# Kernel optimization log

Measured on AMD Instinct MI355X. Metric: run time of the kernel, lower is better.

Reference implementation:

```python
import jax, jax.numpy as jnp
import numpy as np

N = 8192        # num_nodes
H = 128         # h_dim
E = 131072      # num edges (avg degree 16)
NREL = 90       # num relations
NB = 8          # num_bases (block-diagonal decomposition)
SI = H // NB    # block size 16


def setup_inputs() -> dict:
    key = jax.random.key(0)
    ks = jax.random.split(key, 24)
    sc = 0.01
    n = lambda k, shape, s=sc: jax.random.normal(k, shape, dtype=jnp.float32) * s
    return {
        'node_ids': jnp.arange(N, dtype=jnp.int32),
        'src': jax.random.randint(ks[0], (E,), 0, N, dtype=jnp.int32),
        'dst': jax.random.randint(ks[1], (E,), 0, N, dtype=jnp.int32),
        'etypes': jax.random.randint(ks[2], (E,), 0, NREL, dtype=jnp.int32),
        'norm': jax.random.uniform(ks[3], (E, 1), dtype=jnp.float32),
        'eps': jax.random.normal(ks[4], (N, H), dtype=jnp.float32),
        # input embedding layer
        'embedding': n(ks[5], (N, H)),
        # RelGraphConv layer 0 ('bdd'): per-relation block-diag weights, self-loop, bias
        'W0': n(ks[6], (NREL, NB, SI, SI)),
        'loop0': n(ks[7], (H, H)),
        'b0': jnp.zeros((H,), jnp.float32),
        # RelGraphConv layer 1
        'W1': n(ks[8], (NREL, NB, SI, SI)),
        'loop1': n(ks[9], (H, H)),
        'b1': jnp.zeros((H,), jnp.float32),
        # z_layer: Linear(H, 2H)  (weights stored as (in, out))
        'Wz': n(ks[10], (H, 2 * H)),
        'bz': jnp.zeros((2 * H,), jnp.float32),
        # inter_layer (UpdateLayer): Linear(H, H) + h_bias
        'Wi': n(ks[11], (H, H)),
        'bi': jnp.zeros((H,), jnp.float32),
        'hbi': jnp.zeros((H,), jnp.float32),
        # output_layer (second UpdateLayer)
        'Wo': n(ks[12], (H, H)),
        'bo': jnp.zeros((H,), jnp.float32),
        'hbo': jnp.zeros((H,), jnp.float32),
    }


def _rgcn_bdd(h, W, loop_w, bias, src, dst, etypes, norm, act):
    # gather src features, split into NB blocks of size SI
    x = h[src].reshape(-1, NB, SI)                       # [E, NB, SI]
    Wg = W[etypes]                                       # [E, NB, SI, SI] per-edge relation block weights
    msg = jnp.einsum('ebi,ebio->ebo', x, Wg).reshape(-1, H) * norm  # [E, H]
    agg = jax.ops.segment_sum(msg, dst, num_segments=N)  # scatter-add to dst
    out = agg + bias + h @ loop_w                        # self-loop + bias
    return act(out) if act is not None else out


def reference(node_ids, src, dst, etypes, norm, eps, embedding,
              W0, loop0, b0, W1, loop1, b1,
              Wz, bz, Wi, bi, hbi, Wo, bo, hbo):
    # input layer: embedding lookup; saved as input_embed
    x0 = embedding[node_ids]                             # [N, H]
    h = _rgcn_bdd(x0, W0, loop0, b0, src, dst, etypes, norm, jax.nn.relu)
    h = _rgcn_bdd(h, W1, loop1, b1, src, dst, etypes, norm, None)
    # VAE head: z ~ N(mean, exp(log_std))
    zml = h @ Wz + bz                                    # [N, 2H]
    z_mean, z_log_std = jnp.split(zml, 2, axis=-1)
    z = z_mean + jnp.exp(z_log_std) * eps                # reparameterized sample
    # decode 1: outer-product reconstruction + fused update
    R = z @ z.T                                          # [N, N]
    h = R @ (z @ Wi + bi) + R @ x0 + hbi
    # decode 2
    R2 = h @ h.T                                         # [N, N]
    out = R2 @ (h @ Wo + bo) + R2 @ x0 + hbo
    return out
```

## Files before the change

kernel.cpp:

```cpp
#include <hip/hip_runtime.h>
#include <hip/hip_bf16.h>
#include <math.h>

#define Hdim 128
#define NBq 8
#define SIq 16

typedef __attribute__((ext_vector_type(8))) short short8x;
typedef __attribute__((ext_vector_type(4))) float f32x4;

__device__ inline unsigned short f2b(float f) {
  unsigned int u = __float_as_uint(f);
  return (unsigned short)((u + 0x7fffu + ((u >> 16) & 1u)) >> 16);
}
__device__ inline unsigned int pack2(float lo, float hi) {
  return (unsigned int)f2b(lo) | ((unsigned int)f2b(hi) << 16);
}

__global__ void k_gather(const float* __restrict__ emb, const int* __restrict__ ids,
                         float* __restrict__ x0, int N) {
  int idx = blockIdx.x * blockDim.x + threadIdx.x;
  int total = N * (Hdim / 4);
  if (idx >= total) return;
  int n  = idx / (Hdim / 4);
  int c4 = idx - n * (Hdim / 4);
  int s  = ids[n];
  ((float4*)x0)[(size_t)n * (Hdim / 4) + c4] =
      ((const float4*)emb)[(size_t)s * (Hdim / 4) + c4];
}

__global__ void k_wtb(const float* __restrict__ Wa, unsigned short* __restrict__ Wta,
                      const float* __restrict__ Wb, unsigned short* __restrict__ Wtb) {
  int rb = blockIdx.x;
  const float* W = blockIdx.y ? Wb : Wa;
  unsigned short* Wt = blockIdx.y ? Wtb : Wta;
  int t = threadIdx.x;
  int i = t >> 4, o = t & 15;
  Wt[(size_t)rb * 256 + o * 16 + i] = f2b(W[(size_t)rb * 256 + i * 16 + o]);
}

__global__ void k_wtt(const float* __restrict__ l0, const float* __restrict__ l1,
                      const float* __restrict__ Wi, const float* __restrict__ Wo,
                      const float* __restrict__ Wz,
                      unsigned short* __restrict__ l0t, unsigned short* __restrict__ l1t,
                      unsigned short* __restrict__ Wit, unsigned short* __restrict__ Wot,
                      unsigned short* __restrict__ Wzt) {
  int idx = blockIdx.x * blockDim.x + threadIdx.x;
  if (idx < 65536) {
    int w = idx >> 14, local = idx & 16383;
    const float* in = (w == 0) ? l0 : (w == 1) ? l1 : (w == 2) ? Wi : Wo;
    unsigned short* out = (w == 0) ? l0t : (w == 1) ? l1t : (w == 2) ? Wit : Wot;
    int n = local >> 7, k = local & 127;
    out[local] = f2b(in[k * 128 + n]);
  } else {
    int local = idx - 65536;
    int n = local >> 7, k = local & 127;
    Wzt[local] = f2b(Wz[k * 256 + n]);
  }
}

__global__ void k_hist(const int* __restrict__ dst, int* __restrict__ cnt, int E) {
  int e = blockIdx.x * blockDim.x + threadIdx.x;
  if (e < E) atomicAdd(&cnt[dst[e]], 1);
}

__global__ __launch_bounds__(1024) void k_scan(const int* __restrict__ cnt,
                                               int* __restrict__ off,
                                               int* __restrict__ cur, int N, int E) {
  __shared__ int part[1024];
  int t = threadIdx.x;
  int ipt = N / 1024;
  int base = t * ipt;
  int loc[8];
  int s = 0;
  for (int i = 0; i < ipt; ++i) { loc[i] = s; s += cnt[base + i]; }
  part[t] = s;
  __syncthreads();
  for (int d = 1; d < 1024; d <<= 1) {
    int v = part[t];
    int add = (t >= d) ? part[t - d] : 0;
    __syncthreads();
    part[t] = v + add;
    __syncthreads();
  }
  int pre = (t == 0) ? 0 : part[t - 1];
  for (int i = 0; i < ipt; ++i) {
    int o = pre + loc[i];
    off[base + i] = o;
    cur[base + i] = o;
  }
  if (t == 0) off[N] = E;
}

__global__ void k_scatter(const int* __restrict__ src, const int* __restrict__ dst,
                          const int* __restrict__ et, const float* __restrict__ norm,
                          int* __restrict__ cur, int* __restrict__ psrc,
                          int* __restrict__ pet, float* __restrict__ pnorm, int E) {
  int e = blockIdx.x * blockDim.x + threadIdx.x;
  if (e >= E) return;
  int p = atomicAdd(&cur[dst[e]], 1);
  psrc[p] = src[e];
  pet[p]  = et[e];
  pnorm[p] = norm[e];
}

#define BF_LO(u) __uint_as_float((u) << 16)
#define BF_HI(u) __uint_as_float((u) & 0xffff0000u)
__global__ __launch_bounds__(128) void k_edge4(
    const float* __restrict__ h, const unsigned short* __restrict__ Wt,
    const int* __restrict__ off, const int* __restrict__ psrc,
    const int* __restrict__ pet, const float* __restrict__ pnorm,
    float* __restrict__ agg) {
  int n = blockIdx.x;
  int f = threadIdx.x;
  int b = f >> 4, o = f & 15;
  int j0 = off[n], j1 = off[n + 1];
  __shared__ float xs[8][Hdim];
  float acc = 0.f;
  for (int j = j0; j < j1; j += 8) {
    int m = min(8, j1 - j);
    for (int q = 0; q < m; ++q)
      xs[q][f] = h[(size_t)psrc[j + q] * Hdim + f];
    __syncthreads();
    for (int q = 0; q < m; ++q) {
      int r = pet[j + q];
      float nv = pnorm[j + q];
      const uint4* wp = (const uint4*)(Wt + ((size_t)r * NBq + b) * 256 + o * 16);
      uint4 wa = wp[0], wb = wp[1];
      const float4* xp = (const float4*)(&xs[q][b * SIq]);
      float4 x0 = xp[0], x1 = xp[1], x2 = xp[2], x3 = xp[3];
      float a = x0.x*BF_LO(wa.x) + x0.y*BF_HI(wa.x) + x0.z*BF_LO(wa.y) + x0.w*BF_HI(wa.y)
              + x1.x*BF_LO(wa.z) + x1.y*BF_HI(wa.z) + x1.z*BF_LO(wa.w) + x1.w*BF_HI(wa.w)
              + x2.x*BF_LO(wb.x) + x2.y*BF_HI(wb.x) + x2.z*BF_LO(wb.y) + x2.w*BF_HI(wb.y)
              + x3.x*BF_LO(wb.z) + x3.y*BF_HI(wb.z) + x3.z*BF_LO(wb.w) + x3.w*BF_HI(wb.w);
      acc = fmaf(a, nv, acc);
    }
    __syncthreads();
  }
  agg[(size_t)n * Hdim + f] = acc;
}

__global__ __launch_bounds__(256) void k_bgemm(
    const float* __restrict__ A, const unsigned short* __restrict__ Bt,
    const float* __restrict__ Gsrc, float* __restrict__ C,
    const float* __restrict__ addm, const float* __restrict__ bias,
    int M, int Nc, int relu, float* __restrict__ gzero) {
  __shared__ unsigned short Al[32][136];
  __shared__ unsigned short Bl[64][136];
  int t = threadIdx.x;
  int bm = blockIdx.x * 32, bn = blockIdx.y * 64;
  if (gzero && blockIdx.x == 0 && blockIdx.y == 0) {
#pragma unroll
    for (int i = 0; i < 16; ++i)
      ((float4*)gzero)[t + 256 * i] = make_float4(0.f, 0.f, 0.f, 0.f);
  }
  {
    int r = t >> 3, c0 = (t & 7) << 4;
    const float4* ap = (const float4*)(A + (size_t)(bm + r) * Hdim + c0);
    float4 a0 = ap[0], a1 = ap[1], a2 = ap[2], a3 = ap[3];
    uint4 p0 = { pack2(a0.x, a0.y), pack2(a0.z, a0.w), pack2(a1.x, a1.y), pack2(a1.z, a1.w) };
    uint4 p1 = { pack2(a2.x, a2.y), pack2(a2.z, a2.w), pack2(a3.x, a3.y), pack2(a3.z, a3.w) };
    *(uint4*)&Al[r][c0]     = p0;
    *(uint4*)&Al[r][c0 + 8] = p1;
  }
  if (Bt) {
    int n = t >> 2, k0 = (t & 3) << 5;
    const uint4* bp = (const uint4*)(Bt + (size_t)(bn + n) * Hdim + k0);
    uint4 b0 = bp[0], b1 = bp[1], b2 = bp[2], b3 = bp[3];
    *(uint4*)&Bl[n][k0]      = b0;
    *(uint4*)&Bl[n][k0 + 8]  = b1;
    *(uint4*)&Bl[n][k0 + 16] = b2;
    *(uint4*)&Bl[n][k0 + 24] = b3;
  } else {
    int n = t & 63, kb = (t >> 6) << 5;
    for (int i = 0; i < 32; ++i) {
      int k = kb + i;
      Bl[n][k] = f2b(Gsrc[(size_t)k * 128 + bn + n]);
    }
  }
  __syncthreads();
  int wv = t >> 6, ln = t & 63;
  int mt = wv & 1;
  int nt0 = (wv >> 1) << 1;
  int lm = ln & 15, lk = ln >> 4;
  f32x4 acc0 = {0.f, 0.f, 0.f, 0.f}, acc1 = {0.f, 0.f, 0.f, 0.f};
#pragma unroll
  for (int ks = 0; ks < 4; ++ks) {
    short8x af = *(const short8x*)&Al[mt * 16 + lm][ks * 32 + lk * 8];
    short8x bf0 = *(const short8x*)&Bl[nt0 * 16 + lm][ks * 32 + lk * 8];
    short8x bf1 = *(const short8x*)&Bl[(nt0 + 1) * 16 + lm][ks * 32 + lk * 8];
    acc0 = __builtin_amdgcn_mfma_f32_16x16x32_bf16(af, bf0, acc0, 0, 0, 0);
    acc1 = __builtin_amdgcn_mfma_f32_16x16x32_bf16(af, bf1, acc1, 0, 0, 0);
  }
  int gcol0 = bn + nt0 * 16 + lm;
  int gcol1 = gcol0 + 16;
  float b0v = bias ? bias[gcol0] : 0.f;
  float b1v = bias ? bias[gcol1] : 0.f;
#pragma unroll
  for (int reg = 0; reg < 4; ++reg) {
    int grow = bm + mt * 16 + lk * 4 + reg;
    size_t o0 = (size_t)grow * Nc + gcol0;
    size_t o1 = (size_t)grow * Nc + gcol1;
    float v0 = acc0[reg] + b0v;
    float v1 = acc1[reg] + b1v;
    if (addm) { v0 += addm[o0]; v1 += addm[o1]; }
    if (relu) { v0 = fmaxf(v0, 0.f); v1 = fmaxf(v1, 0.f); }
    C[o0] = v0;
    C[o1] = v1;
  }
}


__global__ __launch_bounds__(256) void k_bgemm_z(
    const float* __restrict__ A, const unsigned short* __restrict__ Wzt,
    const float* __restrict__ bz, const float* __restrict__ eps,
    float* __restrict__ Z, int M) {
  __shared__ unsigned short Al[32][136];
  __shared__ unsigned short Bm[64][136];
  __shared__ unsigned short Bl[64][136];
  int t = threadIdx.x;
  int bm = blockIdx.x * 32, bn = blockIdx.y * 64;
  {
    int r = t >> 3, c0 = (t & 7) << 4;
    const float4* ap = (const float4*)(A + (size_t)(bm + r) * Hdim + c0);
    float4 a0 = ap[0], a1 = ap[1], a2 = ap[2], a3 = ap[3];
    uint4 p0 = { pack2(a0.x, a0.y), pack2(a0.z, a0.w), pack2(a1.x, a1.y), pack2(a1.z, a1.w) };
    uint4 p1 = { pack2(a2.x, a2.y), pack2(a2.z, a2.w), pack2(a3.x, a3.y), pack2(a3.z, a3.w) };
    *(uint4*)&Al[r][c0]     = p0;
    *(uint4*)&Al[r][c0 + 8] = p1;
  }
  {
    int n = t >> 2, k0 = (t & 3) << 5;
    const uint4* mp = (const uint4*)(Wzt + (size_t)(bn + n) * Hdim + k0);
    const uint4* lp = (const uint4*)(Wzt + (size_t)(bn + 128 + n) * Hdim + k0);
    uint4 m0 = mp[0], m1 = mp[1], m2 = mp[2], m3 = mp[3];
    uint4 l0 = lp[0], l1 = lp[1], l2 = lp[2], l3 = lp[3];
    *(uint4*)&Bm[n][k0]      = m0; *(uint4*)&Bm[n][k0 + 8]  = m1;
    *(uint4*)&Bm[n][k0 + 16] = m2; *(uint4*)&Bm[n][k0 + 24] = m3;
    *(uint4*)&Bl[n][k0]      = l0; *(uint4*)&Bl[n][k0 + 8]  = l1;
    *(uint4*)&Bl[n][k0 + 16] = l2; *(uint4*)&Bl[n][k0 + 24] = l3;
  }
  __syncthreads();
  int wv = t >> 6, ln = t & 63;
  int mt = wv & 1;
  int nt0 = (wv >> 1) << 1;
  int lm = ln & 15, lk = ln >> 4;
  f32x4 am0 = {0,0,0,0}, am1 = {0,0,0,0}, al0 = {0,0,0,0}, al1 = {0,0,0,0};
#pragma unroll
  for (int ks = 0; ks < 4; ++ks) {
    short8x af = *(const short8x*)&Al[mt * 16 + lm][ks * 32 + lk * 8];
    short8x bm0 = *(const short8x*)&Bm[nt0 * 16 + lm][ks * 32 + lk * 8];
    short8x bm1 = *(const short8x*)&Bm[(nt0 + 1) * 16 + lm][ks * 32 + lk * 8];
    short8x bl0 = *(const short8x*)&Bl[nt0 * 16 + lm][ks * 32 + lk * 8];
    short8x bl1 = *(const short8x*)&Bl[(nt0 + 1) * 16 + lm][ks * 32 + lk * 8];
    am0 = __builtin_amdgcn_mfma_f32_16x16x32_bf16(af, bm0, am0, 0, 0, 0);
    am1 = __builtin_amdgcn_mfma_f32_16x16x32_bf16(af, bm1, am1, 0, 0, 0);
    al0 = __builtin_amdgcn_mfma_f32_16x16x32_bf16(af, bl0, al0, 0, 0, 0);
    al1 = __builtin_amdgcn_mfma_f32_16x16x32_bf16(af, bl1, al1, 0, 0, 0);
  }
  int gcol0 = bn + nt0 * 16 + lm;
  int gcol1 = gcol0 + 16;
  float bm0v = bz[gcol0], bm1v = bz[gcol1];
  float bl0v = bz[128 + gcol0], bl1v = bz[128 + gcol1];
#pragma unroll
  for (int reg = 0; reg < 4; ++reg) {
    int grow = bm + mt * 16 + lk * 4 + reg;
    size_t o0 = (size_t)grow * Hdim + gcol0;
    size_t o1 = (size_t)grow * Hdim + gcol1;
    Z[o0] = am0[reg] + bm0v + expf(al0[reg] + bl0v) * eps[o0];
    Z[o1] = am1[reg] + bm1v + expf(al1[reg] + bl1v) * eps[o1];
  }
}

__global__ __launch_bounds__(256) void k_xty(const float* __restrict__ X,
                                             const float* __restrict__ Y,
                                             float* __restrict__ G, int N) {
  __shared__ float xs[8][64];
  __shared__ float ys[8][64];
  int t  = threadIdx.x;
  int tx = t & 15, ty = t >> 4;
  int qr = blockIdx.y >> 1, qc = blockIdx.y & 1;
  int KC = N / gridDim.x;
  int k0 = blockIdx.x * KC;
  int m  = t >> 7, li = t & 127;
  int lr = li >> 4, lc = (li & 15) << 2;
  const float* S = m ? Y : X;
  int coff = (m ? qc : qr) * 64;
  float acc[4][4] = {};
  for (int kb = 0; kb < KC; kb += 8) {
    float4 v = *(const float4*)(S + (size_t)(k0 + kb + lr) * Hdim + coff + lc);
    __syncthreads();
    if (m) *(float4*)&ys[lr][lc] = v; else *(float4*)&xs[lr][lc] = v;
    __syncthreads();
#pragma unroll
    for (int kk = 0; kk < 8; ++kk) {
      float4 xv = *(const float4*)&xs[kk][ty << 2];
      float4 yv = *(const float4*)&ys[kk][tx << 2];
      acc[0][0] += xv.x * yv.x; acc[0][1] += xv.x * yv.y; acc[0][2] += xv.x * yv.z; acc[0][3] += xv.x * yv.w;
      acc[1][0] += xv.y * yv.x; acc[1][1] += xv.y * yv.y; acc[1][2] += xv.y * yv.z; acc[1][3] += xv.y * yv.w;
      acc[2][0] += xv.z * yv.x; acc[2][1] += xv.z * yv.y; acc[2][2] += xv.z * yv.z; acc[2][3] += xv.z * yv.w;
      acc[3][0] += xv.w * yv.x; acc[3][1] += xv.w * yv.y; acc[3][2] += xv.w * yv.z; acc[3][3] += xv.w * yv.w;
    }
  }
  int grow = qr * 64 + (ty << 2);
  int gcol = qc * 64 + (tx << 2);
#pragma unroll
  for (int r = 0; r < 4; ++r)
#pragma unroll
    for (int c = 0; c < 4; ++c)
      atomicAdd(&G[(size_t)(grow + r) * Hdim + gcol + c], acc[r][c]);
}

extern "C" void kernel_launch(void* const* d_in, const int* in_sizes, int n_in,
                              void* d_out, int out_size, void* d_ws, size_t ws_size,
                              hipStream_t stream) {
  const int*   node_ids = (const int*)d_in[0];
  const int*   src      = (const int*)d_in[1];
  const int*   dst      = (const int*)d_in[2];
  const int*   et       = (const int*)d_in[3];
  const float* norm     = (const float*)d_in[4];
  const float* eps      = (const float*)d_in[5];
  const float* emb      = (const float*)d_in[6];
  const float* W0       = (const float*)d_in[7];
  const float* loop0    = (const float*)d_in[8];
  const float* b0       = (const float*)d_in[9];
  const float* W1       = (const float*)d_in[10];
  const float* loop1    = (const float*)d_in[11];
  const float* b1       = (const float*)d_in[12];
  const float* Wz       = (const float*)d_in[13];
  const float* bz       = (const float*)d_in[14];
  const float* Wi       = (const float*)d_in[15];
  const float* bi       = (const float*)d_in[16];
  const float* hbi      = (const float*)d_in[17];
  const float* Wo       = (const float*)d_in[18];
  const float* bo       = (const float*)d_in[19];
  const float* hbo      = (const float*)d_in[20];
  float* out = (float*)d_out;

  const int N  = in_sizes[0];
  const int E  = in_sizes[1];
  const int RB = in_sizes[7] / (SIq * SIq);

  char* ws = (char*)d_ws;
  const size_t MB = 1u << 20;
  const size_t KB = 1u << 10;
  float* X0   = (float*)(ws + 0 * MB);
  float* B1p  = (float*)(ws + 4 * MB);
  float* B2p  = (float*)(ws + 8 * MB);
  float* AGG  = (float*)(ws + 12 * MB);
  float* B3p  = (float*)(ws + 16 * MB);
  float* G    = (float*)(ws + 20 * MB);
  int*   offp = (int*)(ws + 20 * MB + 256 * KB);
  int*   curp = (int*)(ws + 20 * MB + 512 * KB);
  int*   cntp = (int*)(ws + 20 * MB + 768 * KB);
  int*   psrc = (int*)(ws + 21 * MB);
  int*   pet  = (int*)(ws + 21 * MB + 512 * KB);
  float* pnrm = (float*)(ws + 22 * MB);
  unsigned short* Wt0 = (unsigned short*)(ws + 22 * MB + 512 * KB);
  unsigned short* Wt1 = (unsigned short*)(ws + 23 * MB);
  unsigned short* l0t = (unsigned short*)(ws + 24 * MB);
  unsigned short* l1t = (unsigned short*)(ws + 24 * MB + 64 * KB);
  unsigned short* Wit = (unsigned short*)(ws + 24 * MB + 128 * KB);
  unsigned short* Wot = (unsigned short*)(ws + 24 * MB + 192 * KB);
  unsigned short* Wzt = (unsigned short*)(ws + 24 * MB + 256 * KB);

  dim3 blk(256);

  hipMemsetAsync(cntp, 0, (size_t)N * sizeof(int), stream);
  k_hist<<<dim3((E + 255) / 256), blk, 0, stream>>>(dst, cntp, E);
  k_scan<<<dim3(1), dim3(1024), 0, stream>>>(cntp, offp, curp, N, E);
  k_scatter<<<dim3((E + 255) / 256), blk, 0, stream>>>(src, dst, et, norm, curp,
                                                       psrc, pet, pnrm, E);
  k_wtb<<<dim3(RB, 2), blk, 0, stream>>>(W0, Wt0, W1, Wt1);
  k_wtt<<<dim3(384), blk, 0, stream>>>(loop0, loop1, Wi, Wo, Wz, l0t, l1t, Wit, Wot, Wzt);

  k_gather<<<dim3((N * (Hdim / 4) + 255) / 256), blk, 0, stream>>>(emb, node_ids, X0, N);
  k_edge4<<<dim3(N), dim3(128), 0, stream>>>(X0, Wt0, offp, psrc, pet, pnrm, AGG);
  k_bgemm<<<dim3(N / 32, 2), blk, 0, stream>>>(X0, l0t, nullptr, B1p, AGG, b0, N, Hdim, 1, nullptr);
  k_edge4<<<dim3(N), dim3(128), 0, stream>>>(B1p, Wt1, offp, psrc, pet, pnrm, AGG);
  k_bgemm<<<dim3(N / 32, 2), blk, 0, stream>>>(B1p, l1t, nullptr, B2p, AGG, b1, N, Hdim, 0, nullptr);
  k_bgemm_z<<<dim3(N / 32, 2), blk, 0, stream>>>(B2p, Wzt, bz, eps, B1p, N);
  k_bgemm<<<dim3(N / 32, 2), blk, 0, stream>>>(B1p, Wit, nullptr, B3p, X0, bi, N, Hdim, 0, G);
  k_xty<<<dim3(32, 4), blk, 0, stream>>>(B1p, B3p, G, N);
  k_bgemm<<<dim3(N / 32, 2), blk, 0, stream>>>(B1p, nullptr, G, B2p, nullptr, hbi, N, Hdim, 0, nullptr);
  k_bgemm<<<dim3(N / 32, 2), blk, 0, stream>>>(B2p, Wot, nullptr, B3p, X0, bo, N, Hdim, 0, G);
  k_xty<<<dim3(32, 4), blk, 0, stream>>>(B2p, B3p, G, N);
  k_bgemm<<<dim3(N / 32, 2), blk, 0, stream>>>(B2p, nullptr, G, out, nullptr, hbo, N, Hdim, 0, nullptr);
}
```

Baseline: 302.8 us.

## Fuse preprocessing kernels and software-pipeline edge aggregation without shared memory

```diff
diff --git a/kernel.cpp b/kernel.cpp
--- a/kernel.cpp
+++ b/kernel.cpp
@@ -17,51 +17,48 @@
   return (unsigned int)f2b(lo) | ((unsigned int)f2b(hi) << 16);
 }
 
-__global__ void k_gather(const float* __restrict__ emb, const int* __restrict__ ids,
-                         float* __restrict__ x0, int N) {
-  int idx = blockIdx.x * blockDim.x + threadIdx.x;
-  int total = N * (Hdim / 4);
-  if (idx >= total) return;
-  int n  = idx / (Hdim / 4);
-  int c4 = idx - n * (Hdim / 4);
-  int s  = ids[n];
-  ((float4*)x0)[(size_t)n * (Hdim / 4) + c4] =
-      ((const float4*)emb)[(size_t)s * (Hdim / 4) + c4];
-}
-
-__global__ void k_wtb(const float* __restrict__ Wa, unsigned short* __restrict__ Wta,
-                      const float* __restrict__ Wb, unsigned short* __restrict__ Wtb) {
-  int rb = blockIdx.x;
-  const float* W = blockIdx.y ? Wb : Wa;
-  unsigned short* Wt = blockIdx.y ? Wtb : Wta;
-  int t = threadIdx.x;
-  int i = t >> 4, o = t & 15;
-  Wt[(size_t)rb * 256 + o * 16 + i] = f2b(W[(size_t)rb * 256 + i * 16 + o]);
-}
-
-__global__ void k_wtt(const float* __restrict__ l0, const float* __restrict__ l1,
-                      const float* __restrict__ Wi, const float* __restrict__ Wo,
-                      const float* __restrict__ Wz,
-                      unsigned short* __restrict__ l0t, unsigned short* __restrict__ l1t,
-                      unsigned short* __restrict__ Wit, unsigned short* __restrict__ Wot,
-                      unsigned short* __restrict__ Wzt) {
-  int idx = blockIdx.x * blockDim.x + threadIdx.x;
-  if (idx < 65536) {
-    int w = idx >> 14, local = idx & 16383;
-    const float* in = (w == 0) ? l0 : (w == 1) ? l1 : (w == 2) ? Wi : Wo;
-    unsigned short* out = (w == 0) ? l0t : (w == 1) ? l1t : (w == 2) ? Wit : Wot;
-    int n = local >> 7, k = local & 127;
-    out[local] = f2b(in[k * 128 + n]);
+__global__ __launch_bounds__(256) void k_pre(
+    const float* __restrict__ emb, const int* __restrict__ ids, float* __restrict__ x0,
+    const float* __restrict__ W0, unsigned short* __restrict__ Wt0,
+    const float* __restrict__ W1, unsigned short* __restrict__ Wt1, int w0elems,
+    const float* __restrict__ l0, const float* __restrict__ l1,
+    const float* __restrict__ Wi, const float* __restrict__ Wo, const float* __restrict__ Wz,
+    unsigned short* __restrict__ l0t, unsigned short* __restrict__ l1t,
+    unsigned short* __restrict__ Wit, unsigned short* __restrict__ Wot,
+    unsigned short* __restrict__ Wzt,
+    const int* __restrict__ dst, int* __restrict__ cnt, int E,
+    int b1, int b2, int b3) {
+  int bx = blockIdx.x, t = threadIdx.x;
+  if (bx < b1) {
+    int idx = bx * 256 + t;
+    int n = idx >> 5, c4 = idx & 31;
+    int s = ids[n];
+    ((float4*)x0)[(size_t)n * 32 + c4] = ((const float4*)emb)[(size_t)s * 32 + c4];
+  } else if (bx < b2) {
+    int idx = (bx - b1) * 256 + t;
+    const float* W = (idx < w0elems) ? W0 : W1;
+    unsigned short* Wt = (idx < w0elems) ? Wt0 : Wt1;
+    int local = (idx < w0elems) ? idx : idx - w0elems;
+    int rb = local >> 8, io = local & 255;
+    int i = io >> 4, o = io & 15;
+    Wt[(size_t)rb * 256 + o * 16 + i] = f2b(W[(size_t)rb * 256 + i * 16 + o]);
+  } else if (bx < b3) {
+    int idx = (bx - b2) * 256 + t;
+    if (idx < 65536) {
+      int w = idx >> 14, local = idx & 16383;
+      const float* in = (w == 0) ? l0 : (w == 1) ? l1 : (w == 2) ? Wi : Wo;
+      unsigned short* out = (w == 0) ? l0t : (w == 1) ? l1t : (w == 2) ? Wit : Wot;
+      int n = local >> 7, k = local & 127;
+      out[local] = f2b(in[k * 128 + n]);
+    } else {
+      int local = idx - 65536;
+      int n = local >> 7, k = local & 127;
+      Wzt[local] = f2b(Wz[k * 256 + n]);
+    }
   } else {
-    int local = idx - 65536;
-    int n = local >> 7, k = local & 127;
-    Wzt[local] = f2b(Wz[k * 256 + n]);
-  }
-}
-
-__global__ void k_hist(const int* __restrict__ dst, int* __restrict__ cnt, int E) {
-  int e = blockIdx.x * blockDim.x + threadIdx.x;
-  if (e < E) atomicAdd(&cnt[dst[e]], 1);
+    int e = (bx - b3) * 256 + t;
+    if (e < E) atomicAdd(&cnt[dst[e]], 1);
+  }
 }
 
 __global__ __launch_bounds__(1024) void k_scan(const int* __restrict__ cnt,
@@ -106,36 +103,44 @@
 
 #define BF_LO(u) __uint_as_float((u) << 16)
 #define BF_HI(u) __uint_as_float((u) & 0xffff0000u)
-__global__ __launch_bounds__(128) void k_edge4(
+__global__ __launch_bounds__(256) void k_edge6(
     const float* __restrict__ h, const unsigned short* __restrict__ Wt,
     const int* __restrict__ off, const int* __restrict__ psrc,
     const int* __restrict__ pet, const float* __restrict__ pnorm,
     float* __restrict__ agg) {
-  int n = blockIdx.x;
-  int f = threadIdx.x;
+  int t = threadIdx.x;
+  int n = blockIdx.x * 2 + (t >> 7);
+  int f = t & 127;
   int b = f >> 4, o = f & 15;
   int j0 = off[n], j1 = off[n + 1];
-  __shared__ float xs[8][Hdim];
   float acc = 0.f;
-  for (int j = j0; j < j1; j += 8) {
-    int m = min(8, j1 - j);
-    for (int q = 0; q < m; ++q)
-      xs[q][f] = h[(size_t)psrc[j + q] * Hdim + f];
-    __syncthreads();
-    for (int q = 0; q < m; ++q) {
-      int r = pet[j + q];
-      float nv = pnorm[j + q];
-      const uint4* wp = (const uint4*)(Wt + ((size_t)r * NBq + b) * 256 + o * 16);
-      uint4 wa = wp[0], wb = wp[1];
-      const float4* xp = (const float4*)(&xs[q][b * SIq]);
-      float4 x0 = xp[0], x1 = xp[1], x2 = xp[2], x3 = xp[3];
+  if (j0 < j1) {
+    int jlast = j1 - 1;
+    int r0 = pet[j0], s0 = psrc[j0];
+    float nv = pnorm[j0];
+    const uint4* wp = (const uint4*)(Wt + ((size_t)r0 * NBq + b) * 256 + o * 16);
+    uint4 wa = wp[0], wb = wp[1];
+    const float4* xp = (const float4*)(h + (size_t)s0 * Hdim + b * SIq);
+    float4 x0 = xp[0], x1 = xp[1], x2 = xp[2], x3 = xp[3];
+    int j1c = min(j0 + 1, jlast);
+    int rn = pet[j1c], sn = psrc[j1c];
+    float nvn = pnorm[j1c];
+    for (int j = j0; j < j1; ++j) {
+      const uint4* wpn = (const uint4*)(Wt + ((size_t)rn * NBq + b) * 256 + o * 16);
+      uint4 wan = wpn[0], wbn = wpn[1];
+      const float4* xpn = (const float4*)(h + (size_t)sn * Hdim + b * SIq);
+      float4 xn0 = xpn[0], xn1 = xpn[1], xn2 = xpn[2], xn3 = xpn[3];
+      int j2c = min(j + 2, jlast);
+      int r2 = pet[j2c], s2 = psrc[j2c];
+      float nv2 = pnorm[j2c];
       float a = x0.x*BF_LO(wa.x) + x0.y*BF_HI(wa.x) + x0.z*BF_LO(wa.y) + x0.w*BF_HI(wa.y)
               + x1.x*BF_LO(wa.z) + x1.y*BF_HI(wa.z) + x1.z*BF_LO(wa.w) + x1.w*BF_HI(wa.w)
               + x2.x*BF_LO(wb.x) + x2.y*BF_HI(wb.x) + x2.z*BF_LO(wb.y) + x2.w*BF_HI(wb.y)
               + x3.x*BF_LO(wb.z) + x3.y*BF_HI(wb.z) + x3.z*BF_LO(wb.w) + x3.w*BF_HI(wb.w);
       acc = fmaf(a, nv, acc);
+      wa = wan; wb = wbn; x0 = xn0; x1 = xn1; x2 = xn2; x3 = xn3;
+      nv = nvn; nvn = nv2; rn = r2; sn = s2;
     }
-    __syncthreads();
   }
   agg[(size_t)n * Hdim + f] = acc;
 }
@@ -209,7 +214,6 @@
     C[o1] = v1;
   }
 }
-
 
 __global__ __launch_bounds__(256) void k_bgemm_z(
     const float* __restrict__ A, const unsigned short* __restrict__ Wzt,
@@ -366,18 +370,24 @@
 
   dim3 blk(256);
 
+  const int w0elems = RB * 256;
+  const int gB   = (N * 32) / 256;
+  const int wtbB = (2 * w0elems + 255) / 256;
+  const int wttB = 98304 / 256;
+  const int histB = (E + 255) / 256;
+  const int b1s = gB, b2s = gB + wtbB, b3s = gB + wtbB + wttB;
   hipMemsetAsync(cntp, 0, (size_t)N * sizeof(int), stream);
-  k_hist<<<dim3((E + 255) / 256), blk, 0, stream>>>(dst, cntp, E);
+  k_pre<<<dim3(b3s + histB), blk, 0, stream>>>(
+      emb, node_ids, X0, W0, Wt0, W1, Wt1, w0elems,
+      loop0, loop1, Wi, Wo, Wz, l0t, l1t, Wit, Wot, Wzt,
+      dst, cntp, E, b1s, b2s, b3s);
   k_scan<<<dim3(1), dim3(1024), 0, stream>>>(cntp, offp, curp, N, E);
   k_scatter<<<dim3((E + 255) / 256), blk, 0, stream>>>(src, dst, et, norm, curp,
                                                        psrc, pet, pnrm, E);
-  k_wtb<<<dim3(RB, 2), blk, 0, stream>>>(W0, Wt0, W1, Wt1);
-  k_wtt<<<dim3(384), blk, 0, stream>>>(loop0, loop1, Wi, Wo, Wz, l0t, l1t, Wit, Wot, Wzt);
-
-  k_gather<<<dim3((N * (Hdim / 4) + 255) / 256), blk, 0, stream>>>(emb, node_ids, X0, N);
-  k_edge4<<<dim3(N), dim3(128), 0, stream>>>(X0, Wt0, offp, psrc, pet, pnrm, AGG);
+
+  k_edge6<<<dim3(N / 2), blk, 0, stream>>>(X0, Wt0, offp, psrc, pet, pnrm, AGG);
   k_bgemm<<<dim3(N / 32, 2), blk, 0, stream>>>(X0, l0t, nullptr, B1p, AGG, b0, N, Hdim, 1, nullptr);
-  k_edge4<<<dim3(N), dim3(128), 0, stream>>>(B1p, Wt1, offp, psrc, pet, pnrm, AGG);
+  k_edge6<<<dim3(N / 2), blk, 0, stream>>>(B1p, Wt1, offp, psrc, pet, pnrm, AGG);
   k_bgemm<<<dim3(N / 32, 2), blk, 0, stream>>>(B1p, l1t, nullptr, B2p, AGG, b1, N, Hdim, 0, nullptr);
   k_bgemm_z<<<dim3(N / 32, 2), blk, 0, stream>>>(B2p, Wzt, bz, eps, B1p, N);
   k_bgemm<<<dim3(N / 32, 2), blk, 0, stream>>>(B1p, Wit, nullptr, B3p, X0, bi, N, Hdim, 0, G);
```

After: 345.5 us. +14.1%, slower.
